# Kernel tuning notes

Hardware: AMD Instinct MI355X
Metric: run time of the kernel (lower is better)

## Reference

```python
import jax, jax.numpy as jnp
import numpy as np

# Dims: N tokens, D input, H expert hidden, O output, E experts, G gate hidden, K top-k
N, D, H, O, E, G, K = 8192, 1024, 2048, 1024, 8, 256, 2
BALANCE_COEF = 0.01


def setup_inputs() -> dict:
    key = jax.random.key(0)
    ks = jax.random.split(key, 12)
    def lin(k, shape, fan_in):
        return jax.random.normal(k, shape, jnp.float32) * (1.0 / np.sqrt(fan_in))
    return {
        "x":   jax.random.normal(ks[0], (N, D), jnp.float32),
        # gating MLP: D -> G -> E
        "Wg1": lin(ks[1], (D, G), D), "bg1": jnp.zeros((G,), jnp.float32),
        "Wg2": lin(ks[2], (G, E), G), "bg2": jnp.zeros((E,), jnp.float32),
        # stacked expert MLPs: D -> H -> H -> O (ExpertNetwork, num_layers=2)
        "W1": lin(ks[3], (E, D, H), D), "b1": jnp.zeros((E, H), jnp.float32),
        "W2": lin(ks[4], (E, H, H), H), "b2": jnp.zeros((E, H), jnp.float32),
        "W3": lin(ks[5], (E, H, O), H), "b3": jnp.zeros((E, O), jnp.float32),
    }


def reference(x, Wg1, bg1, Wg2, bg2, W1, b1, W2, b2, W3, b3):
    # Gating: 2-layer MLP -> softmax -> top-k -> renormalize (eval: no noise/dropout)
    logits = jnp.maximum(x @ Wg1 + bg1, 0.0) @ Wg2 + bg2            # [N, E]
    probs = jax.nn.softmax(logits, axis=-1)
    w, idx = jax.lax.top_k(probs, K)                                # [N, K]
    w = w / jnp.sum(w, axis=-1, keepdims=True)
    onehot = jax.nn.one_hot(idx, E, dtype=x.dtype)                  # [N, K, E]
    comb = jnp.sum(onehot * w[..., None], axis=1)                   # [N, E] per-token expert weight

    # Dense-equivalent combine: unselected tokens get weight 0, identical math to
    # the masked dispatch + scatter-add in the torch code.
    def expert_step(acc, params):
        W1e, b1e, W2e, b2e, W3e, b3e, we = params                   # we: [N]
        h = jnp.maximum(x @ W1e + b1e, 0.0)                         # [N, H]
        h = jnp.maximum(h @ W2e + b2e, 0.0)                         # [N, H]
        o = h @ W3e + b3e                                           # [N, O]
        return acc + o * we[:, None], None

    out, _ = jax.lax.scan(expert_step, jnp.zeros((N, O), x.dtype),
                          (W1, b1, W2, b2, W3, b3, comb.T))

    # aux losses: expert_usage[e] = sum_i mean_b(indices[b,i]==e)
    expert_usage = jnp.sum(onehot, axis=(0, 1)) / N                 # [E]
    balance_loss = jnp.mean((expert_usage - 1.0 / E) ** 2) * BALANCE_COEF
    return out, balance_loss, expert_usage
```

## Files before the change

kernel.cpp:

```cpp
#include <hip/hip_runtime.h>
#include <hip/hip_bf16.h>
#include <cstdint>
#include <cstddef>

#define N_TOK 8192
#define D_IN  1024
#define H_DIM 2048
#define O_DIM 1024
#define E_NUM 8
#define G_DIM 256
#define MAXTILES 136
#define MAXROWS  (MAXTILES*128)

typedef __attribute__((ext_vector_type(8))) __bf16 bf16x8;
typedef __attribute__((ext_vector_type(4))) float floatx4;

#define GCAST(p) ((__attribute__((address_space(1))) void*)(void*)(p))
#define LCAST(p) ((__attribute__((address_space(3))) void*)(p))

#define JOB_G1_END   512
#define JOB_CAST_END 4608
#define JOB_W1_END   8704

__device__ inline void transpose_body(const float* __restrict__ src,
                                      __bf16* __restrict__ dst,
                                      int K, int N, int e, int ktile, int ntile,
                                      float* smemf) {
  float (*tl)[64] = (float(*)[64])smemf;
  const float* s = src + (size_t)e * K * N;
  __bf16* d = dst + (size_t)e * K * N;
  int k0 = ktile * 64, n0 = ntile * 64;
  int t = threadIdx.x;
  int kr = t >> 4, nc = t & 15;
#pragma unroll
  for (int p = 0; p < 4; p++) {
    int r = kr + p * 16;
    float4 v = *reinterpret_cast<const float4*>(
        s + (size_t)(k0 + r) * N + n0 + nc * 4);
    *reinterpret_cast<float4*>(&tl[r][(nc * 4 + 8 * (r >> 3)) & 63]) = v;
  }
  __syncthreads();
  int n = t >> 3, kg = t & 7;
#pragma unroll
  for (int p = 0; p < 2; p++) {
    int c = n + p * 32;
    bf16x8 o;
#pragma unroll
    for (int j = 0; j < 8; j++)
      o[j] = (__bf16)tl[kg * 8 + j][(c + 8 * kg) & 63];
    *reinterpret_cast<bf16x8*>(d + (size_t)(n0 + c) * K + k0 + kg * 8) = o;
  }
}

__device__ inline void gate1_body(const float* __restrict__ x,
                                  const float* __restrict__ Wg1,
                                  const float* __restrict__ bg1,
                                  float* __restrict__ g,
                                  int bn, int bm, float* smemf) {
  float (*As)[68] = (float(*)[68])smemf;
  float (*Bs)[68] = (float(*)[68])(smemf + 32 * 68);
  int t = threadIdx.x;
  int tm = t >> 4, tn = t & 15;
  float acc[4][4] = {};
  for (int k0 = 0; k0 < D_IN; k0 += 32) {
#pragma unroll
    for (int i = 0; i < 2; i++) {
      int idx = t + 256 * i;
      int row = idx >> 3, c4 = idx & 7;
      float4 v = *reinterpret_cast<const float4*>(
          x + (size_t)(bm * 64 + row) * D_IN + k0 + c4 * 4);
      As[c4 * 4 + 0][row] = v.x;
      As[c4 * 4 + 1][row] = v.y;
      As[c4 * 4 + 2][row] = v.z;
      As[c4 * 4 + 3][row] = v.w;
      int brow = idx >> 4, bc4 = idx & 15;
      float4 wv = *reinterpret_cast<const float4*>(
          Wg1 + (size_t)(k0 + brow) * G_DIM + bn * 64 + bc4 * 4);
      *reinterpret_cast<float4*>(&Bs[brow][bc4 * 4]) = wv;
    }
    __syncthreads();
#pragma unroll
    for (int k = 0; k < 32; k++) {
      float4 av = *reinterpret_cast<const float4*>(&As[k][tm * 4]);
      float4 bv = *reinterpret_cast<const float4*>(&Bs[k][tn * 4]);
      float a4[4] = {av.x, av.y, av.z, av.w};
      float b4[4] = {bv.x, bv.y, bv.z, bv.w};
#pragma unroll
      for (int r = 0; r < 4; r++)
#pragma unroll
        for (int c = 0; c < 4; c++) acc[r][c] = fmaf(a4[r], b4[c], acc[r][c]);
    }
    __syncthreads();
  }
  int gr = bm * 64 + tm * 4, gc = bn * 64 + tn * 4;
#pragma unroll
  for (int r = 0; r < 4; r++) {
    float4 o;
    o.x = fmaxf(acc[r][0] + bg1[gc + 0], 0.f);
    o.y = fmaxf(acc[r][1] + bg1[gc + 1], 0.f);
    o.z = fmaxf(acc[r][2] + bg1[gc + 2], 0.f);
    o.w = fmaxf(acc[r][3] + bg1[gc + 3], 0.f);
    *reinterpret_cast<float4*>(g + (size_t)(gr + r) * G_DIM + gc) = o;
  }
}

__global__ __launch_bounds__(256) void prep_kernel(
    const float* __restrict__ x, __bf16* __restrict__ xb,
    const float* __restrict__ W1, __bf16* __restrict__ W1t,
    const float* __restrict__ Wg1, const float* __restrict__ bg1,
    float* __restrict__ g) {
  __shared__ float smemf[4352];
  int b = blockIdx.x;
  if (b < JOB_G1_END) {
    gate1_body(x, Wg1, bg1, g, b & 3, b >> 2, smemf);
  } else if (b < JOB_CAST_END) {
    int id = b - JOB_G1_END;
    int i = id * 2048 + threadIdx.x * 8;
    float4 v0 = *reinterpret_cast<const float4*>(x + i);
    float4 v1 = *reinterpret_cast<const float4*>(x + i + 4);
    bf16x8 o;
    o[0] = (__bf16)v0.x; o[1] = (__bf16)v0.y; o[2] = (__bf16)v0.z; o[3] = (__bf16)v0.w;
    o[4] = (__bf16)v1.x; o[5] = (__bf16)v1.y; o[6] = (__bf16)v1.z; o[7] = (__bf16)v1.w;
    *reinterpret_cast<bf16x8*>(xb + i) = o;
  } else {
    int id = b - JOB_CAST_END;
    transpose_body(W1, W1t, D_IN, H_DIM, id >> 9, (id >> 5) & 15, id & 31, smemf);
  }
}

__global__ __launch_bounds__(256) void gate2_kernel(const float* __restrict__ g,
                                                    const float* __restrict__ Wg2,
                                                    const float* __restrict__ bg2,
                                                    int* __restrict__ top_idx,
                                                    float* __restrict__ top_w,
                                                    int* __restrict__ counts) {
  __shared__ float lg[32][9];
  int t = threadIdx.x;
  int tl = t >> 3, e = t & 7;
  int n = blockIdx.x * 32 + tl;
  const float* gr = g + (size_t)n * G_DIM;
  float acc = bg2[e];
  for (int i = 0; i < G_DIM; i += 4) {
    float4 v = *reinterpret_cast<const float4*>(gr + i);
    acc += v.x * Wg2[(i + 0) * E_NUM + e];
    acc += v.y * Wg2[(i + 1) * E_NUM + e];
    acc += v.z * Wg2[(i + 2) * E_NUM + e];
    acc += v.w * Wg2[(i + 3) * E_NUM + e];
  }
  lg[tl][e] = acc;
  __syncthreads();
  if (e == 0) {
    float l[8];
#pragma unroll
    for (int i = 0; i < 8; i++) l[i] = lg[tl][i];
    int i0 = 0;
    for (int i = 1; i < 8; i++)
      if (l[i] > l[i0]) i0 = i;
    int i1 = (i0 == 0) ? 1 : 0;
    for (int i = 0; i < 8; i++)
      if (i != i0 && l[i] > l[i1]) i1 = i;
    float d = expf(l[i1] - l[i0]);
    float w0 = 1.f / (1.f + d);
    float w1 = d * w0;
    top_idx[n * 2 + 0] = i0;
    top_idx[n * 2 + 1] = i1;
    top_w[n * 2 + 0] = w0;
    top_w[n * 2 + 1] = w1;
    atomicAdd(&counts[i0], 1);
    atomicAdd(&counts[i1], 1);
  }
}

__global__ void g3_kernel(const int* __restrict__ counts, int* __restrict__ cursors,
                          int* __restrict__ off_pad, int* __restrict__ ntiles,
                          int* __restrict__ tile_meta, float* __restrict__ out_tail,
                          int* __restrict__ slot_token) {
  if (threadIdx.x == 0) {
    int off = 0, nt = 0;
    float mse = 0.f;
    for (int e = 0; e < E_NUM; e++) {
      off_pad[e] = off;
      int c = counts[e];
      int tiles = (c + 127) >> 7;
      for (int i = 0; i < tiles; i++) {
        tile_meta[nt * 2 + 0] = e;
        tile_meta[nt * 2 + 1] = off + i * 128;
        nt++;
      }
      off += tiles << 7;
      cursors[e] = 0;
      float u = (float)c / (float)N_TOK;
      out_tail[1 + e] = u;
      float dd = u - 0.125f;
      mse += dd * dd;
    }
    *ntiles = nt;
    out_tail[0] = (mse / 8.0f) * 0.01f;
  }
  for (int s = threadIdx.x; s < MAXROWS; s += 256) slot_token[s] = 0;
}

__global__ __launch_bounds__(256) void scatter_kernel(const int* __restrict__ top_idx,
                                                      const int* __restrict__ off_pad,
                                                      int* __restrict__ cursors,
                                                      int* __restrict__ slot_token,
                                                      int* __restrict__ token_slots) {
  int n = blockIdx.x * 256 + threadIdx.x;
#pragma unroll
  for (int k = 0; k < 2; k++) {
    int e = top_idx[n * 2 + k];
    int pos = atomicAdd(&cursors[e], 1);
    int s = off_pad[e] + pos;
    slot_token[s] = n;
    token_slots[n * 2 + k] = s;
  }
}

__global__ __launch_bounds__(256) void moe_gemm_kernel(
    const __bf16* __restrict__ A, int Astride, int gatherA,
    const __bf16* __restrict__ Wt, const float* __restrict__ bias,
    int Kdim, int Ndim,
    const int* __restrict__ tile_meta, const int* __restrict__ ntiles_p,
    const int* __restrict__ slot_token,
    __bf16* __restrict__ h_out, float* __restrict__ y_out, int finalMode,
    const float* __restrict__ W2src, __bf16* __restrict__ W2dst,
    const float* __restrict__ W3src, __bf16* __restrict__ W3dst) {
  __shared__ __align__(16) char smem[32768];
  int tile = blockIdx.y;
  if (tile >= MAXTILES) {
    int id = (tile - MAXTILES) * gridDim.x + blockIdx.x;
    if (id < 8192) {
      transpose_body(W2src, W2dst, H_DIM, H_DIM, id >> 10, (id >> 5) & 31,
                     id & 31, (float*)smem);
    } else {
      id -= 8192;
      transpose_body(W3src, W3dst, H_DIM, O_DIM, id >> 9, (id >> 4) & 31,
                     id & 15, (float*)smem);
    }
    return;
  }
  if (tile >= *ntiles_p) return;
  __bf16* As = (__bf16*)smem;
  __bf16* Bs = (__bf16*)(smem + 16384);
  int ex = tile_meta[tile * 2 + 0];
  int slot0 = tile_meta[tile * 2 + 1];
  int n0 = blockIdx.x * 128;
  int t = threadIdx.x, l = t & 63, w = t >> 6;

  size_t aoff[4], boff[4];
#pragma unroll
  for (int i = 0; i < 4; i++) {
    int gidx = (w * 4 + i) * 64 + l;
    int row = gidx >> 3;
    int kch = (gidx & 7) ^ (row & 7);
    int sl = slot0 + row;
    long long rb = gatherA ? (long long)slot_token[sl] * Astride
                           : (long long)sl * Astride;
    aoff[i] = (size_t)rb + kch * 8;
    boff[i] = ((size_t)ex * Ndim + n0 + row) * (size_t)Kdim + kch * 8;
  }

  int wm = (w >> 1) * 64, wn = (w & 1) * 64;
  int lm = l & 15, lq = l >> 4;
  floatx4 acc[4][4] = {};

  for (int k0 = 0; k0 < Kdim; k0 += 64) {
#pragma unroll
    for (int i = 0; i < 4; i++) {
      __builtin_amdgcn_global_load_lds(GCAST(A + aoff[i] + k0),
                                       LCAST((char*)As + w * 4096 + i * 1024),
                                       16, 0, 0);
      __builtin_amdgcn_global_load_lds(GCAST(Wt + boff[i] + k0),
                                       LCAST((char*)Bs + w * 4096 + i * 1024),
                                       16, 0, 0);
    }
    __syncthreads();
#pragma unroll
    for (int half = 0; half < 2; half++) {
      bf16x8 af[4], bfr[4];
#pragma unroll
      for (int i = 0; i < 4; i++) {
        int r = wm + i * 16 + lm;
        int s = (half * 4 + lq) ^ (r & 7);
        af[i] = *reinterpret_cast<const bf16x8*>(As + r * 64 + s * 8);
      }
#pragma unroll
      for (int j = 0; j < 4; j++) {
        int r = wn + j * 16 + lm;
        int s = (half * 4 + lq) ^ (r & 7);
        bfr[j] = *reinterpret_cast<const bf16x8*>(Bs + r * 64 + s * 8);
      }
#pragma unroll
      for (int i = 0; i < 4; i++)
#pragma unroll
        for (int j = 0; j < 4; j++)
          acc[i][j] = __builtin_amdgcn_mfma_f32_16x16x32_bf16(af[i], bfr[j],
                                                              acc[i][j], 0, 0, 0);
    }
    __syncthreads();
  }

  float bcol[4];
#pragma unroll
  for (int j = 0; j < 4; j++) bcol[j] = bias[(size_t)ex * Ndim + n0 + wn + j * 16 + lm];

  if (finalMode) {
#pragma unroll
    for (int i = 0; i < 4; i++) {
#pragma unroll
      for (int r = 0; r < 4; r++) {
        int sl = slot0 + wm + i * 16 + lq * 4 + r;
        float* yrow = y_out + (size_t)sl * Ndim + n0 + wn + lm;
#pragma unroll
        for (int j = 0; j < 4; j++) yrow[j * 16] = acc[i][j][r] + bcol[j];
      }
    }
  } else {
#pragma unroll
    for (int i = 0; i < 4; i++) {
#pragma unroll
      for (int r = 0; r < 4; r++) {
        int sl = slot0 + wm + i * 16 + lq * 4 + r;
        __bf16* hrow = h_out + (size_t)sl * Ndim + n0 + wn + lm;
#pragma unroll
        for (int j = 0; j < 4; j++) {
          float v = fmaxf(acc[i][j][r] + bcol[j], 0.f);
          hrow[j * 16] = (__bf16)v;
        }
      }
    }
  }
}

__global__ __launch_bounds__(256) void combine_kernel(const float* __restrict__ y,
                                                      const int* __restrict__ token_slots,
                                                      const float* __restrict__ top_w,
                                                      float* __restrict__ out) {
  int n = blockIdx.x;
  int t = threadIdx.x;
  int s0 = token_slots[n * 2 + 0], s1 = token_slots[n * 2 + 1];
  float w0 = top_w[n * 2 + 0], w1 = top_w[n * 2 + 1];
  float4 a = reinterpret_cast<const float4*>(y + (size_t)s0 * O_DIM)[t];
  float4 b = reinterpret_cast<const float4*>(y + (size_t)s1 * O_DIM)[t];
  float4 o;
  o.x = w0 * a.x + w1 * b.x;
  o.y = w0 * a.y + w1 * b.y;
  o.z = w0 * a.z + w1 * b.z;
  o.w = w0 * a.w + w1 * b.w;
  reinterpret_cast<float4*>(out + (size_t)n * O_DIM)[t] = o;
}

extern "C" void kernel_launch(void* const* d_in, const int* in_sizes, int n_in,
                              void* d_out, int out_size, void* d_ws, size_t ws_size,
                              hipStream_t stream) {
  const float* x   = (const float*)d_in[0];
  const float* Wg1 = (const float*)d_in[1];
  const float* bg1 = (const float*)d_in[2];
  const float* Wg2 = (const float*)d_in[3];
  const float* bg2 = (const float*)d_in[4];
  const float* W1  = (const float*)d_in[5];
  const float* b1  = (const float*)d_in[6];
  const float* W2  = (const float*)d_in[7];
  const float* b2  = (const float*)d_in[8];
  const float* W3  = (const float*)d_in[9];
  const float* b3  = (const float*)d_in[10];
  float* out = (float*)d_out;

  char* ws = (char*)d_ws;
  __bf16* x_bf       = (__bf16*)(ws + 0);
  __bf16* W1t        = (__bf16*)(ws + 16777216);
  __bf16* W2t        = (__bf16*)(ws + 50331648);
  __bf16* W3t        = (__bf16*)(ws + 117440512);
  __bf16* h1         = (__bf16*)(ws + 150994944);
  __bf16* h2         = (__bf16*)(ws + 222298112);
  float*  y          = (float*) (ws + 150994944);
  float*  gbuf       = (float*) (ws + 293601280);
  int*    top_idx    = (int*)   (ws + 301989888);
  float*  top_w      = (float*) (ws + 302055424);
  int*    slot_token = (int*)   (ws + 302120960);
  int*    token_slots= (int*)   (ws + 302190592);
  int*    meta       = (int*)   (ws + 302260224);
  int* counts    = meta;
  int* cursors   = meta + 8;
  int* off_pad   = meta + 16;
  int* ntiles    = meta + 24;
  int* tile_meta = meta + 32;
  float* out_tail = out + (size_t)N_TOK * O_DIM;

  hipMemsetAsync(meta, 0, 64, stream);

  prep_kernel<<<JOB_W1_END, 256, 0, stream>>>(x, x_bf, W1, W1t, Wg1, bg1, gbuf);
  gate2_kernel<<<N_TOK / 32, 256, 0, stream>>>(gbuf, Wg2, bg2, top_idx, top_w, counts);
  g3_kernel<<<1, 256, 0, stream>>>(counts, cursors, off_pad, ntiles, tile_meta, out_tail,
                                   slot_token);
  scatter_kernel<<<N_TOK / 256, 256, 0, stream>>>(top_idx, off_pad, cursors,
                                                  slot_token, token_slots);

  moe_gemm_kernel<<<dim3(H_DIM / 128, MAXTILES + 768), 256, 0, stream>>>(
      x_bf, D_IN, 1, W1t, b1, D_IN, H_DIM, tile_meta, ntiles, slot_token,
      h1, nullptr, 0, W2, W2t, W3, W3t);
  moe_gemm_kernel<<<dim3(H_DIM / 128, MAXTILES), 256, 0, stream>>>(
      h1, H_DIM, 0, W2t, b2, H_DIM, H_DIM, tile_meta, ntiles, slot_token,
      h2, nullptr, 0, nullptr, nullptr, nullptr, nullptr);
  moe_gemm_kernel<<<dim3(O_DIM / 128, MAXTILES), 256, 0, stream>>>(
      h2, H_DIM, 0, W3t, b3, H_DIM, O_DIM, tile_meta, ntiles, slot_token,
      nullptr, y, 1, nullptr, nullptr, nullptr, nullptr);
  combine_kernel<<<N_TOK, 256, 0, stream>>>(y, token_slots, top_w, out);
}
```

Before: 944.6 us.

## Triple-buffer LDS with async global-to-LDS prefetch in MoE GEMM

```diff
diff --git a/kernel.cpp b/kernel.cpp
--- a/kernel.cpp
+++ b/kernel.cpp
@@ -225,7 +225,7 @@
     __bf16* __restrict__ h_out, float* __restrict__ y_out, int finalMode,
     const float* __restrict__ W2src, __bf16* __restrict__ W2dst,
     const float* __restrict__ W3src, __bf16* __restrict__ W3dst) {
-  __shared__ __align__(16) char smem[32768];
+  __shared__ __align__(16) char smem[49152];
   int tile = blockIdx.y;
   if (tile >= MAXTILES) {
     int id = (tile - MAXTILES) * gridDim.x + blockIdx.x;
@@ -240,19 +240,17 @@
     return;
   }
   if (tile >= *ntiles_p) return;
-  __bf16* As = (__bf16*)smem;
-  __bf16* Bs = (__bf16*)(smem + 16384);
   int ex = tile_meta[tile * 2 + 0];
   int slot0 = tile_meta[tile * 2 + 1];
   int n0 = blockIdx.x * 128;
   int t = threadIdx.x, l = t & 63, w = t >> 6;
 
-  size_t aoff[4], boff[4];
-#pragma unroll
-  for (int i = 0; i < 4; i++) {
-    int gidx = (w * 4 + i) * 64 + l;
-    int row = gidx >> 3;
-    int kch = (gidx & 7) ^ (row & 7);
+  size_t aoff[2], boff[2];
+#pragma unroll
+  for (int i = 0; i < 2; i++) {
+    int gidx = i * 256 + t;
+    int row = gidx >> 2;
+    int kch = (gidx & 3) ^ (row & 3);
     int sl = slot0 + row;
     long long rb = gatherA ? (long long)slot_token[sl] * Astride
                            : (long long)sl * Astride;
@@ -264,41 +262,68 @@
   int lm = l & 15, lq = l >> 4;
   floatx4 acc[4][4] = {};
 
-  for (int k0 = 0; k0 < Kdim; k0 += 64) {
+  auto STAGEF = [&](int h, int b) {
+    char* Ab = smem + b * 16384;
+#pragma unroll
+    for (int i = 0; i < 2; i++) {
+      __builtin_amdgcn_global_load_lds(GCAST(A + aoff[i] + h * 32),
+                                       LCAST(Ab + i * 4096 + w * 1024), 16, 0, 0);
+      __builtin_amdgcn_global_load_lds(GCAST(Wt + boff[i] + h * 32),
+                                       LCAST(Ab + 8192 + i * 4096 + w * 1024), 16, 0, 0);
+    }
+  };
+  auto COMPUTEF = [&](int b) {
+    const __bf16* As = (const __bf16*)(smem + b * 16384);
+    const __bf16* Bs = As + 4096;
+    bf16x8 af[4], bfr[4];
 #pragma unroll
     for (int i = 0; i < 4; i++) {
-      __builtin_amdgcn_global_load_lds(GCAST(A + aoff[i] + k0),
-                                       LCAST((char*)As + w * 4096 + i * 1024),
-                                       16, 0, 0);
-      __builtin_amdgcn_global_load_lds(GCAST(Wt + boff[i] + k0),
-                                       LCAST((char*)Bs + w * 4096 + i * 1024),
-                                       16, 0, 0);
-    }
-    __syncthreads();
-#pragma unroll
-    for (int half = 0; half < 2; half++) {
-      bf16x8 af[4], bfr[4];
-#pragma unroll
-      for (int i = 0; i < 4; i++) {
-        int r = wm + i * 16 + lm;
-        int s = (half * 4 + lq) ^ (r & 7);
-        af[i] = *reinterpret_cast<const bf16x8*>(As + r * 64 + s * 8);
-      }
-#pragma unroll
-      for (int j = 0; j < 4; j++) {
-        int r = wn + j * 16 + lm;
-        int s = (half * 4 + lq) ^ (r & 7);
-        bfr[j] = *reinterpret_cast<const bf16x8*>(Bs + r * 64 + s * 8);
-      }
-#pragma unroll
-      for (int i = 0; i < 4; i++)
-#pragma unroll
-        for (int j = 0; j < 4; j++)
-          acc[i][j] = __builtin_amdgcn_mfma_f32_16x16x32_bf16(af[i], bfr[j],
-                                                              acc[i][j], 0, 0, 0);
-    }
-    __syncthreads();
-  }
+      int r = wm + i * 16 + lm;
+      af[i] = *reinterpret_cast<const bf16x8*>(As + r * 32 + (lq ^ (r & 3)) * 8);
+    }
+#pragma unroll
+    for (int j = 0; j < 4; j++) {
+      int r = wn + j * 16 + lm;
+      bfr[j] = *reinterpret_cast<const bf16x8*>(Bs + r * 32 + (lq ^ (r & 3)) * 8);
+    }
+    __builtin_amdgcn_s_setprio(1);
+#pragma unroll
+    for (int i = 0; i < 4; i++)
+#pragma unroll
+      for (int j = 0; j < 4; j++)
+        acc[i][j] = __builtin_amdgcn_mfma_f32_16x16x32_bf16(af[i], bfr[j],
+                                                            acc[i][j], 0, 0, 0);
+    __builtin_amdgcn_s_setprio(0);
+  };
+
+  int nh = Kdim >> 5;
+
+  asm volatile("s_waitcnt vmcnt(0)" ::: "memory");
+  STAGEF(0, 0);
+  STAGEF(1, 1);
+  STAGEF(2, 2);
+
+  int b = 0;
+  for (int h = 0; h < nh - 2; ++h) {
+    asm volatile("s_waitcnt vmcnt(8)" ::: "memory");
+    __builtin_amdgcn_s_barrier();
+    __builtin_amdgcn_sched_barrier(0);
+    COMPUTEF(b);
+    asm volatile("s_waitcnt lgkmcnt(0)" ::: "memory");
+    __builtin_amdgcn_s_barrier();
+    __builtin_amdgcn_sched_barrier(0);
+    if (h + 3 < nh) STAGEF(h + 3, b);
+    b = (b == 2) ? 0 : b + 1;
+  }
+  asm volatile("s_waitcnt vmcnt(4)" ::: "memory");
+  __builtin_amdgcn_s_barrier();
+  __builtin_amdgcn_sched_barrier(0);
+  COMPUTEF(b);
+  b = (b == 2) ? 0 : b + 1;
+  asm volatile("s_waitcnt vmcnt(0)" ::: "memory");
+  __builtin_amdgcn_s_barrier();
+  __builtin_amdgcn_sched_barrier(0);
+  COMPUTEF(b);
 
   float bcol[4];
 #pragma unroll
```

After: 1.018 ms. +7.7%, slower.

## Double-buffer MoE GEMM with 512-thread 128x256 tiles and batched transposes

Applied to the files above, without the earlier changes.

```diff
diff --git a/kernel.cpp b/kernel.cpp
--- a/kernel.cpp
+++ b/kernel.cpp
@@ -50,6 +50,32 @@
       o[j] = (__bf16)tl[kg * 8 + j][(c + 8 * kg) & 63];
     *reinterpret_cast<bf16x8*>(d + (size_t)(n0 + c) * K + k0 + kg * 8) = o;
   }
+}
+
+__device__ inline void transpose_body512(const float* __restrict__ src,
+                                         __bf16* __restrict__ dst,
+                                         int K, int N, int e, int ktile, int ntile,
+                                         float* smemf) {
+  float (*tl)[64] = (float(*)[64])smemf;
+  const float* s = src + (size_t)e * K * N;
+  __bf16* d = dst + (size_t)e * K * N;
+  int k0 = ktile * 64, n0 = ntile * 64;
+  int t = threadIdx.x;
+  int kr = t >> 4, nc = t & 15;
+#pragma unroll
+  for (int p = 0; p < 2; p++) {
+    int r = kr + p * 32;
+    float4 v = *reinterpret_cast<const float4*>(
+        s + (size_t)(k0 + r) * N + n0 + nc * 4);
+    *reinterpret_cast<float4*>(&tl[r][(nc * 4 + 8 * (r >> 3)) & 63]) = v;
+  }
+  __syncthreads();
+  int n = t >> 3, kg = t & 7;
+  bf16x8 o;
+#pragma unroll
+  for (int j = 0; j < 8; j++)
+    o[j] = (__bf16)tl[kg * 8 + j][(n + 8 * kg) & 63];
+  *reinterpret_cast<bf16x8*>(d + (size_t)(n0 + n) * K + k0 + kg * 8) = o;
 }
 
 __device__ inline void gate1_body(const float* __restrict__ x,
@@ -216,7 +242,7 @@
   }
 }
 
-__global__ __launch_bounds__(256) void moe_gemm_kernel(
+__global__ __launch_bounds__(512) void moe_gemm_kernel(
     const __bf16* __restrict__ A, int Astride, int gatherA,
     const __bf16* __restrict__ Wt, const float* __restrict__ bias,
     int Kdim, int Ndim,
@@ -225,79 +251,112 @@
     __bf16* __restrict__ h_out, float* __restrict__ y_out, int finalMode,
     const float* __restrict__ W2src, __bf16* __restrict__ W2dst,
     const float* __restrict__ W3src, __bf16* __restrict__ W3dst) {
-  __shared__ __align__(16) char smem[32768];
+  __shared__ __align__(16) char smem[98304];
   int tile = blockIdx.y;
+  int t = threadIdx.x;
   if (tile >= MAXTILES) {
-    int id = (tile - MAXTILES) * gridDim.x + blockIdx.x;
-    if (id < 8192) {
-      transpose_body(W2src, W2dst, H_DIM, H_DIM, id >> 10, (id >> 5) & 31,
-                     id & 31, (float*)smem);
-    } else {
-      id -= 8192;
-      transpose_body(W3src, W3dst, H_DIM, O_DIM, id >> 9, (id >> 4) & 31,
-                     id & 15, (float*)smem);
+    int id16 = (tile - MAXTILES) * gridDim.x + blockIdx.x;
+#pragma unroll 1
+    for (int it = 0; it < 16; ++it) {
+      int id = id16 * 16 + it;
+      if (id < 8192) {
+        transpose_body512(W2src, W2dst, H_DIM, H_DIM, id >> 10, (id >> 5) & 31,
+                          id & 31, (float*)smem);
+      } else {
+        int id3 = id - 8192;
+        transpose_body512(W3src, W3dst, H_DIM, O_DIM, id3 >> 9, (id3 >> 4) & 31,
+                          id3 & 15, (float*)smem);
+      }
+      __syncthreads();
     }
     return;
   }
   if (tile >= *ntiles_p) return;
-  __bf16* As = (__bf16*)smem;
-  __bf16* Bs = (__bf16*)(smem + 16384);
   int ex = tile_meta[tile * 2 + 0];
   int slot0 = tile_meta[tile * 2 + 1];
-  int n0 = blockIdx.x * 128;
-  int t = threadIdx.x, l = t & 63, w = t >> 6;
-
-  size_t aoff[4], boff[4];
-#pragma unroll
-  for (int i = 0; i < 4; i++) {
-    int gidx = (w * 4 + i) * 64 + l;
+  int n0 = blockIdx.x * 256;
+  int l = t & 63, w = t >> 6;
+
+  size_t aoff[2], boff[4];
+#pragma unroll
+  for (int i = 0; i < 2; i++) {
+    int gidx = i * 512 + t;
     int row = gidx >> 3;
     int kch = (gidx & 7) ^ (row & 7);
     int sl = slot0 + row;
     long long rb = gatherA ? (long long)slot_token[sl] * Astride
                            : (long long)sl * Astride;
     aoff[i] = (size_t)rb + kch * 8;
+  }
+#pragma unroll
+  for (int i = 0; i < 4; i++) {
+    int gidx = i * 512 + t;
+    int row = gidx >> 3;
+    int kch = (gidx & 7) ^ (row & 7);
     boff[i] = ((size_t)ex * Ndim + n0 + row) * (size_t)Kdim + kch * 8;
   }
 
-  int wm = (w >> 1) * 64, wn = (w & 1) * 64;
+  int wm = (w >> 2) * 64, wn = (w & 3) * 64;
   int lm = l & 15, lq = l >> 4;
   floatx4 acc[4][4] = {};
 
-  for (int k0 = 0; k0 < Kdim; k0 += 64) {
-#pragma unroll
-    for (int i = 0; i < 4; i++) {
-      __builtin_amdgcn_global_load_lds(GCAST(A + aoff[i] + k0),
-                                       LCAST((char*)As + w * 4096 + i * 1024),
-                                       16, 0, 0);
-      __builtin_amdgcn_global_load_lds(GCAST(Wt + boff[i] + k0),
-                                       LCAST((char*)Bs + w * 4096 + i * 1024),
-                                       16, 0, 0);
-    }
-    __syncthreads();
-#pragma unroll
-    for (int half = 0; half < 2; half++) {
+  auto STAGE = [&](int kt, int b) {
+    char* base = smem + b * 49152;
+#pragma unroll
+    for (int i = 0; i < 2; i++)
+      __builtin_amdgcn_global_load_lds(GCAST(A + aoff[i] + kt * 64),
+                                       LCAST(base + i * 8192 + w * 1024), 16, 0, 0);
+#pragma unroll
+    for (int i = 0; i < 4; i++)
+      __builtin_amdgcn_global_load_lds(GCAST(Wt + boff[i] + kt * 64),
+                                       LCAST(base + 16384 + i * 8192 + w * 1024), 16, 0, 0);
+  };
+  auto COMPUTE = [&](int b) {
+    const __bf16* As = (const __bf16*)(smem + b * 49152);
+    const __bf16* Bs = As + 8192;
+#pragma unroll
+    for (int ks = 0; ks < 2; ks++) {
       bf16x8 af[4], bfr[4];
 #pragma unroll
       for (int i = 0; i < 4; i++) {
         int r = wm + i * 16 + lm;
-        int s = (half * 4 + lq) ^ (r & 7);
-        af[i] = *reinterpret_cast<const bf16x8*>(As + r * 64 + s * 8);
+        af[i] = *reinterpret_cast<const bf16x8*>(As + r * 64 + ((ks * 4 + lq) ^ (r & 7)) * 8);
       }
 #pragma unroll
       for (int j = 0; j < 4; j++) {
-        int r = wn + j * 16 + lm;
-        int s = (half * 4 + lq) ^ (r & 7);
-        bfr[j] = *reinterpret_cast<const bf16x8*>(Bs + r * 64 + s * 8);
-      }
+        int c = wn + j * 16 + lm;
+        bfr[j] = *reinterpret_cast<const bf16x8*>(Bs + c * 64 + ((ks * 4 + lq) ^ (c & 7)) * 8);
+      }
+      __builtin_amdgcn_s_setprio(1);
 #pragma unroll
       for (int i = 0; i < 4; i++)
 #pragma unroll
         for (int j = 0; j < 4; j++)
           acc[i][j] = __builtin_amdgcn_mfma_f32_16x16x32_bf16(af[i], bfr[j],
                                                               acc[i][j], 0, 0, 0);
-    }
-    __syncthreads();
+      __builtin_amdgcn_s_setprio(0);
+    }
+  };
+
+  int NKT = Kdim >> 6;
+
+  asm volatile("s_waitcnt vmcnt(0)" ::: "memory");
+  STAGE(0, 0);
+#pragma unroll 1
+  for (int kt = 0; kt < NKT; ++kt) {
+    int d = kt & 1;
+    if (kt + 1 < NKT) {
+      STAGE(kt + 1, d ^ 1);
+      asm volatile("s_waitcnt vmcnt(6)" ::: "memory");
+    } else {
+      asm volatile("s_waitcnt vmcnt(0)" ::: "memory");
+    }
+    __builtin_amdgcn_s_barrier();
+    __builtin_amdgcn_sched_barrier(0);
+    COMPUTE(d);
+    asm volatile("s_waitcnt lgkmcnt(0)" ::: "memory");
+    __builtin_amdgcn_s_barrier();
+    __builtin_amdgcn_sched_barrier(0);
   }
 
   float bcol[4];
@@ -396,13 +455,13 @@
   scatter_kernel<<<N_TOK / 256, 256, 0, stream>>>(top_idx, off_pad, cursors,
                                                   slot_token, token_slots);
 
-  moe_gemm_kernel<<<dim3(H_DIM / 128, MAXTILES + 768), 256, 0, stream>>>(
+  moe_gemm_kernel<<<dim3(H_DIM / 256, MAXTILES + 96), 512, 0, stream>>>(
       x_bf, D_IN, 1, W1t, b1, D_IN, H_DIM, tile_meta, ntiles, slot_token,
       h1, nullptr, 0, W2, W2t, W3, W3t);
-  moe_gemm_kernel<<<dim3(H_DIM / 128, MAXTILES), 256, 0, stream>>>(
+  moe_gemm_kernel<<<dim3(H_DIM / 256, MAXTILES), 512, 0, stream>>>(
       h1, H_DIM, 0, W2t, b2, H_DIM, H_DIM, tile_meta, ntiles, slot_token,
       h2, nullptr, 0, nullptr, nullptr, nullptr, nullptr);
-  moe_gemm_kernel<<<dim3(O_DIM / 128, MAXTILES), 256, 0, stream>>>(
+  moe_gemm_kernel<<<dim3(O_DIM / 256, MAXTILES), 512, 0, stream>>>(
       h2, H_DIM, 0, W3t, b3, H_DIM, O_DIM, tile_meta, ntiles, slot_token,
       nullptr, y, 1, nullptr, nullptr, nullptr, nullptr);
   combine_kernel<<<N_TOK, 256, 0, stream>>>(y, token_slots, top_w, out);
```

Result: slower. 1.031 ms (+9.1%).

## Widen MoE GEMM tile to 128x256 with each wave owning full M rows

Applied to the files above, without the earlier changes.

```diff
diff --git a/kernel.cpp b/kernel.cpp
--- a/kernel.cpp
+++ b/kernel.cpp
@@ -216,7 +216,7 @@
   }
 }
 
-__global__ __launch_bounds__(256) void moe_gemm_kernel(
+__global__ __launch_bounds__(256, 2) void moe_gemm_kernel(
     const __bf16* __restrict__ A, int Astride, int gatherA,
     const __bf16* __restrict__ Wt, const float* __restrict__ bias,
     int Kdim, int Ndim,
@@ -225,7 +225,7 @@
     __bf16* __restrict__ h_out, float* __restrict__ y_out, int finalMode,
     const float* __restrict__ W2src, __bf16* __restrict__ W2dst,
     const float* __restrict__ W3src, __bf16* __restrict__ W3dst) {
-  __shared__ __align__(16) char smem[32768];
+  __shared__ __align__(16) char smem[49152];
   int tile = blockIdx.y;
   if (tile >= MAXTILES) {
     int id = (tile - MAXTILES) * gridDim.x + blockIdx.x;
@@ -244,54 +244,59 @@
   __bf16* Bs = (__bf16*)(smem + 16384);
   int ex = tile_meta[tile * 2 + 0];
   int slot0 = tile_meta[tile * 2 + 1];
-  int n0 = blockIdx.x * 128;
+  int n0 = blockIdx.x * 256;
   int t = threadIdx.x, l = t & 63, w = t >> 6;
 
-  size_t aoff[4], boff[4];
+  size_t aoff[4], boff[8];
 #pragma unroll
   for (int i = 0; i < 4; i++) {
-    int gidx = (w * 4 + i) * 64 + l;
+    int gidx = i * 256 + t;
     int row = gidx >> 3;
     int kch = (gidx & 7) ^ (row & 7);
     int sl = slot0 + row;
     long long rb = gatherA ? (long long)slot_token[sl] * Astride
                            : (long long)sl * Astride;
     aoff[i] = (size_t)rb + kch * 8;
+  }
+#pragma unroll
+  for (int i = 0; i < 8; i++) {
+    int gidx = i * 256 + t;
+    int row = gidx >> 3;
+    int kch = (gidx & 7) ^ (row & 7);
     boff[i] = ((size_t)ex * Ndim + n0 + row) * (size_t)Kdim + kch * 8;
   }
 
-  int wm = (w >> 1) * 64, wn = (w & 1) * 64;
+  int wn = w * 64;
   int lm = l & 15, lq = l >> 4;
-  floatx4 acc[4][4] = {};
+  floatx4 acc[8][4] = {};
 
   for (int k0 = 0; k0 < Kdim; k0 += 64) {
 #pragma unroll
-    for (int i = 0; i < 4; i++) {
+    for (int i = 0; i < 4; i++)
       __builtin_amdgcn_global_load_lds(GCAST(A + aoff[i] + k0),
-                                       LCAST((char*)As + w * 4096 + i * 1024),
+                                       LCAST((char*)As + i * 4096 + w * 1024),
                                        16, 0, 0);
+#pragma unroll
+    for (int i = 0; i < 8; i++)
       __builtin_amdgcn_global_load_lds(GCAST(Wt + boff[i] + k0),
-                                       LCAST((char*)Bs + w * 4096 + i * 1024),
+                                       LCAST((char*)Bs + i * 4096 + w * 1024),
                                        16, 0, 0);
-    }
     __syncthreads();
 #pragma unroll
-    for (int half = 0; half < 2; half++) {
-      bf16x8 af[4], bfr[4];
-#pragma unroll
-      for (int i = 0; i < 4; i++) {
-        int r = wm + i * 16 + lm;
-        int s = (half * 4 + lq) ^ (r & 7);
-        af[i] = *reinterpret_cast<const bf16x8*>(As + r * 64 + s * 8);
+    for (int ks = 0; ks < 2; ks++) {
+      bf16x8 af[8], bfr[4];
+#pragma unroll
+      for (int i = 0; i < 8; i++) {
+        int r = i * 16 + lm;
+        af[i] = *reinterpret_cast<const bf16x8*>(As + r * 64 + ((ks * 4 + lq) ^ (r & 7)) * 8);
       }
 #pragma unroll
       for (int j = 0; j < 4; j++) {
-        int r = wn + j * 16 + lm;
-        int s = (half * 4 + lq) ^ (r & 7);
-        bfr[j] = *reinterpret_cast<const bf16x8*>(Bs + r * 64 + s * 8);
+        int c = wn + j * 16 + lm;
+        bfr[j] = *reinterpret_cast<const bf16x8*>(Bs + c * 64 + ((ks * 4 + lq) ^ (c & 7)) * 8);
       }
 #pragma unroll
-      for (int i = 0; i < 4; i++)
+      for (int i = 0; i < 8; i++)
 #pragma unroll
         for (int j = 0; j < 4; j++)
           acc[i][j] = __builtin_amdgcn_mfma_f32_16x16x32_bf16(af[i], bfr[j],
@@ -306,10 +311,10 @@
 
   if (finalMode) {
 #pragma unroll
-    for (int i = 0; i < 4; i++) {
+    for (int i = 0; i < 8; i++) {
 #pragma unroll
       for (int r = 0; r < 4; r++) {
-        int sl = slot0 + wm + i * 16 + lq * 4 + r;
+        int sl = slot0 + i * 16 + lq * 4 + r;
         float* yrow = y_out + (size_t)sl * Ndim + n0 + wn + lm;
 #pragma unroll
         for (int j = 0; j < 4; j++) yrow[j * 16] = acc[i][j][r] + bcol[j];
@@ -317,10 +322,10 @@
     }
   } else {
 #pragma unroll
-    for (int i = 0; i < 4; i++) {
+    for (int i = 0; i < 8; i++) {
 #pragma unroll
       for (int r = 0; r < 4; r++) {
-        int sl = slot0 + wm + i * 16 + lq * 4 + r;
+        int sl = slot0 + i * 16 + lq * 4 + r;
         __bf16* hrow = h_out + (size_t)sl * Ndim + n0 + wn + lm;
 #pragma unroll
         for (int j = 0; j < 4; j++) {
@@ -396,13 +401,13 @@
   scatter_kernel<<<N_TOK / 256, 256, 0, stream>>>(top_idx, off_pad, cursors,
                                                   slot_token, token_slots);
 
-  moe_gemm_kernel<<<dim3(H_DIM / 128, MAXTILES + 768), 256, 0, stream>>>(
+  moe_gemm_kernel<<<dim3(H_DIM / 256, MAXTILES + 1536), 256, 0, stream>>>(
       x_bf, D_IN, 1, W1t, b1, D_IN, H_DIM, tile_meta, ntiles, slot_token,
       h1, nullptr, 0, W2, W2t, W3, W3t);
-  moe_gemm_kernel<<<dim3(H_DIM / 128, MAXTILES), 256, 0, stream>>>(
+  moe_gemm_kernel<<<dim3(H_DIM / 256, MAXTILES), 256, 0, stream>>>(
       h1, H_DIM, 0, W2t, b2, H_DIM, H_DIM, tile_meta, ntiles, slot_token,
       h2, nullptr, 0, nullptr, nullptr, nullptr, nullptr);
-  moe_gemm_kernel<<<dim3(O_DIM / 128, MAXTILES), 256, 0, stream>>>(
+  moe_gemm_kernel<<<dim3(O_DIM / 256, MAXTILES), 256, 0, stream>>>(
       h2, H_DIM, 0, W3t, b3, H_DIM, O_DIM, tile_meta, ntiles, slot_token,
       nullptr, y, 1, nullptr, nullptr, nullptr, nullptr);
   combine_kernel<<<N_TOK, 256, 0, stream>>>(y, token_slots, top_w, out);
```

New measurement: 994.6 us. 1.05x slower.
